# Kernel tuning notes

Hardware: AMD Instinct MI355X
Metric: run time of the kernel (lower is better)

Reference implementation:

```python
import math
import jax, jax.numpy as jnp
import numpy as np

D = 1024
NH = 16
DH = D // NH


def setup_inputs() -> dict:
    key = jax.random.key(0)
    k1, k2, k3 = jax.random.split(key, 3)
    x = jax.random.normal(k1, (2, 2048, D), dtype=jnp.float32)
    s = 1.0 / math.sqrt(D)
    W_qkv = jax.random.normal(k2, (D, 3 * D), dtype=jnp.float32) * s
    W_o = jax.random.normal(k3, (D, D), dtype=jnp.float32) * s
    return {"x": x, "W_qkv": W_qkv, "W_o": W_o}


def _rope(q, k, base=10000.0):
    # q, k: [B, H, T, dh]
    half = q.shape[-1] // 2
    freqs = jnp.arange(half, dtype=q.dtype) / half
    theta = 1.0 / base ** freqs                      # [half]
    t = jnp.arange(q.shape[-2], dtype=q.dtype)       # [T]
    ang = t[:, None] * theta[None, :]                # [T, half]
    cos = jnp.cos(ang)[None, None, :, :]
    sin = jnp.sin(ang)[None, None, :, :]

    def rot(x):
        x1, x2 = x[..., :half], x[..., half:]
        return jnp.concatenate([x1 * cos - x2 * sin, x1 * sin + x2 * cos], axis=-1)

    return rot(q), rot(k)


def reference(x, W_qkv, W_o):
    B, T, d = x.shape
    qkv = x @ W_qkv                                   # [B, T, 3D]
    q, k, v = jnp.split(qkv, 3, axis=-1)
    q = q.reshape(B, T, NH, DH).transpose(0, 2, 1, 3)  # [B, H, T, dh]
    k = k.reshape(B, T, NH, DH).transpose(0, 2, 1, 3)
    v = v.reshape(B, T, NH, DH).transpose(0, 2, 1, 3)
    q, k = _rope(q, k)
    att = jnp.einsum('bhtd,bhsd->bhts', q, k) / math.sqrt(DH)  # [B, H, T, T]
    mask = jnp.triu(jnp.full((T, T), -jnp.inf, dtype=att.dtype), 1)
    att = att + mask
    w = jax.nn.softmax(att, axis=-1)
    y = jnp.einsum('bhts,bhsd->bhtd', w, v)           # [B, H, T, dh]
    y = y.transpose(0, 2, 1, 3).reshape(B, T, d)
    return y @ W_o
```

## Files before the change

### kernel.cpp

```cpp
#include <hip/hip_runtime.h>

typedef __bf16 bf16x8 __attribute__((ext_vector_type(8)));
typedef float f32x4 __attribute__((ext_vector_type(4)));
typedef float f32x16 __attribute__((ext_vector_type(16)));

constexpr int SEQ = 2048;
constexpr int DMODEL = 1024;

#define GLL(gp, lp)                                                              \
  __builtin_amdgcn_global_load_lds((const __attribute__((address_space(1))) void*)(gp), \
                                   (__attribute__((address_space(3))) void*)(lp), 16, 0, 0)

__global__ __launch_bounds__(256) void prep_kernel(const float* __restrict__ x,
                                                   const float* __restrict__ Wqkv,
                                                   const float* __restrict__ Wo,
                                                   __bf16* __restrict__ xbf,
                                                   __bf16* __restrict__ WqkvT,
                                                   __bf16* __restrict__ WoT,
                                                   float2* __restrict__ sct) {
  __shared__ __bf16 tile[64][72];
  int blk = blockIdx.x, t = threadIdx.x;

  if (blk < 256) {
    int i = blk * 256 + t;
    int tt = i >> 5, j = i & 31;
    float theta = exp2f(-(float)j * 0.41524101186092953f);
    float s, c;
    __sincosf((float)tt * theta, &s, &c);
    sct[i] = make_float2(c, s);
    return;
  }
  if (blk >= 1280) {
    size_t i = (size_t)(blk - 1280) * 256 + t;
    const float* sp = x + i * 8;
    float4 f0 = *reinterpret_cast<const float4*>(sp);
    float4 f1 = *reinterpret_cast<const float4*>(sp + 4);
    alignas(16) __bf16 tmp[8];
    tmp[0] = (__bf16)f0.x; tmp[1] = (__bf16)f0.y; tmp[2] = (__bf16)f0.z; tmp[3] = (__bf16)f0.w;
    tmp[4] = (__bf16)f1.x; tmp[5] = (__bf16)f1.y; tmp[6] = (__bf16)f1.z; tmp[7] = (__bf16)f1.w;
    *reinterpret_cast<uint4*>(xbf + i * 8) = *reinterpret_cast<const uint4*>(tmp);
    return;
  }
  const float* src;
  __bf16* dst;
  int C, R, c0, r0;
  if (blk < 512) {
    int idx = blk - 256;
    src = Wo; dst = WoT; R = 1024; C = 1024;
    c0 = (idx & 15) * 64; r0 = (idx >> 4) * 64;
  } else {
    int idx = blk - 512;
    src = Wqkv; dst = WqkvT; R = 1024; C = 3072;
    c0 = (idx % 48) * 64; r0 = (idx / 48) * 64;
  }
#pragma unroll
  for (int p = 0; p < 2; ++p) {
    int flat = p * 256 + t;
    int i = flat >> 3;
    int j8 = (flat & 7) * 8;
    const float* sp = &src[(size_t)(r0 + i) * C + c0 + j8];
    float4 f0 = *reinterpret_cast<const float4*>(sp);
    float4 f1 = *reinterpret_cast<const float4*>(sp + 4);
    tile[i][j8 + 0] = (__bf16)f0.x; tile[i][j8 + 1] = (__bf16)f0.y;
    tile[i][j8 + 2] = (__bf16)f0.z; tile[i][j8 + 3] = (__bf16)f0.w;
    tile[i][j8 + 4] = (__bf16)f1.x; tile[i][j8 + 5] = (__bf16)f1.y;
    tile[i][j8 + 6] = (__bf16)f1.z; tile[i][j8 + 7] = (__bf16)f1.w;
  }
  __syncthreads();
#pragma unroll
  for (int p = 0; p < 2; ++p) {
    int flat = p * 256 + t;
    int i = flat >> 3;
    int j8 = (flat & 7) * 8;
    alignas(16) __bf16 tmp[8];
#pragma unroll
    for (int jj = 0; jj < 8; ++jj) tmp[jj] = tile[j8 + jj][i];
    *reinterpret_cast<uint4*>(&dst[(size_t)(c0 + i) * R + r0 + j8]) =
        *reinterpret_cast<const uint4*>(tmp);
  }
}

__global__ __launch_bounds__(256) void transpose_v(const __bf16* __restrict__ qkv,
                                                   __bf16* __restrict__ vt) {
  __shared__ __bf16 tile[64][72];
  int s0 = blockIdx.x * 64;
  int bh = blockIdx.y;
  int b = bh >> 4, h = bh & 15;
  const __bf16* src = qkv + (size_t)b * SEQ * 3072 + 2048 + h * 64;
  __bf16* dst = vt + (size_t)bh * 64 * SEQ;
  int t = threadIdx.x;
#pragma unroll
  for (int p = 0; p < 2; ++p) {
    int flat = p * 256 + t;
    int i = flat >> 3;
    int j8 = (flat & 7) * 8;
    *reinterpret_cast<uint4*>(&tile[i][j8]) =
        *reinterpret_cast<const uint4*>(src + (size_t)(s0 + i) * 3072 + j8);
  }
  __syncthreads();
#pragma unroll
  for (int p = 0; p < 2; ++p) {
    int flat = p * 256 + t;
    int i = flat >> 3;
    int j8 = (flat & 7) * 8;
    alignas(16) __bf16 tmp[8];
#pragma unroll
    for (int jj = 0; jj < 8; ++jj) tmp[jj] = tile[j8 + jj][i];
    *reinterpret_cast<uint4*>(dst + (size_t)i * SEQ + s0 + j8) =
        *reinterpret_cast<const uint4*>(tmp);
  }
}

template <typename CT, int BN, int MODE>
__global__ __launch_bounds__(256) void gemm_bt_lds(const __bf16* __restrict__ A,
                                                   const __bf16* __restrict__ BT,
                                                   CT* __restrict__ C,
                                                   int M, int N, int K, int lda, int ldc,
                                                   const float2* __restrict__ sct) {
  constexpr int MF = (BN == 128) ? 4 : 2;
  __shared__ __align__(16) __bf16 A_lds[128][64];
  __shared__ __align__(16) __bf16 B_lds[BN][64];
  int tid = threadIdx.x;
  int lane = tid & 63, w = tid >> 6;
  int g = lane >> 4, l15 = lane & 15;
  int wr = (BN == 128) ? (w >> 1) : w;
  int wc = (BN == 128) ? (w & 1) : 0;
  int m0 = blockIdx.x * 128;
  int n0 = blockIdx.y * BN;
  int srow = lane >> 3, scol = (lane & 7) * 8;

  const __bf16* ag = A + (size_t)(m0 + w * 32 + srow) * lda + scol;
  const __bf16* bg = BT + (size_t)(n0 + w * (BN / 4) + srow) * K + scol;

  f32x4 acc[MF][4] = {};

  for (int k0 = 0; k0 < K; k0 += 64) {
    __syncthreads();
#pragma unroll
    for (int i = 0; i < 4; ++i)
      GLL(ag + (size_t)(i * 8) * lda + k0, &A_lds[w * 32 + i * 8][0]);
#pragma unroll
    for (int i = 0; i < BN / 32; ++i)
      GLL(bg + (size_t)(i * 8) * K + k0, &B_lds[w * (BN / 4) + i * 8][0]);
    __syncthreads();
#pragma unroll
    for (int kk = 0; kk < 2; ++kk) {
      bf16x8 a[MF], bb[4];
#pragma unroll
      for (int m = 0; m < MF; ++m)
        a[m] = *reinterpret_cast<const bf16x8*>(&A_lds[wr * (MF * 16) + m * 16 + l15][kk * 32 + g * 8]);
#pragma unroll
      for (int n = 0; n < 4; ++n)
        bb[n] = *reinterpret_cast<const bf16x8*>(&B_lds[wc * 64 + n * 16 + l15][kk * 32 + g * 8]);
#pragma unroll
      for (int m = 0; m < MF; ++m)
#pragma unroll
        for (int n = 0; n < 4; ++n)
          acc[m][n] = __builtin_amdgcn_mfma_f32_16x16x32_bf16(a[m], bb[n], acc[m][n], 0, 0, 0);
    }
  }

  if constexpr (MODE == 1) {
    bool isq = (n0 < 1024), isk = (n0 >= 1024 && n0 < 2048);
    if (isq || isk) {
      float sc = isq ? 0.18033688011112042f : 1.0f;
#pragma unroll
      for (int m = 0; m < MF; ++m)
#pragma unroll
        for (int r = 0; r < 4; ++r) {
          int row = m0 + wr * (MF * 16) + m * 16 + 4 * g + r;
          int t = row & (SEQ - 1);
#pragma unroll
          for (int n = 0; n < 2; ++n) {
            int j = n * 16 + l15;
            float2 cs = sct[(t << 5) + j];
            float x1 = acc[m][n][r], x2 = acc[m][n + 2][r];
            acc[m][n][r]     = (x1 * cs.x - x2 * cs.y) * sc;
            acc[m][n + 2][r] = (x1 * cs.y + x2 * cs.x) * sc;
          }
        }
    }
  }

#pragma unroll
  for (int m = 0; m < MF; ++m)
#pragma unroll
    for (int n = 0; n < 4; ++n)
#pragma unroll
      for (int r = 0; r < 4; ++r) {
        int row = m0 + wr * (MF * 16) + m * 16 + 4 * g + r;
        int col = n0 + wc * 64 + n * 16 + l15;
        C[(size_t)row * ldc + col] = (CT)acc[m][n][r];
      }
}

__device__ inline uint32_t pkbf(float a, float b) {
  union { __bf16 h[2]; uint32_t u; } z;
  z.h[0] = (__bf16)a; z.h[1] = (__bf16)b;
  return z.u;
}

__global__ __launch_bounds__(128, 3) void attn_kernel(__bf16* __restrict__ qkv,
                                                      const __bf16* __restrict__ vt,
                                                      float* __restrict__ pml) {
  __shared__ __align__(16) __bf16 K_lds[2][64][64];

  int tid = threadIdx.x;
  int w = tid >> 6, lane = tid & 63;
  int l31 = lane & 31, hi = lane >> 5;
  int bid = blockIdx.x;
  int it = bid >> 5, bh = bid & 31;
  int b = bh >> 4, h = bh & 15;

  int qc, kv0, kv1, half;
  bool split;
  if (it < 32) {
    qc = 31 - (it >> 1);
    half = it & 1;
    int NTf = qc + 1;
    int hs = (NTf + 1) >> 1;
    kv0 = half ? hs : 0;
    kv1 = half ? NTf : hs;
    split = true;
  } else {
    qc = 47 - it;
    kv0 = 0;
    kv1 = qc + 1;
    split = false;
    half = 0;
  }
  int NT = kv1 - kv0;

  __bf16* qbase = qkv + (size_t)b * SEQ * 3072 + h * 64;
  const __bf16* kbase = qbase + 1024;
  const __bf16* vtb = vt + (size_t)bh * 64 * SEQ;

  int q_g = qc * 64 + w * 32 + l31;

  int r8 = lane >> 3;
  int cxe = 8 * ((lane & 7) ^ r8);

  auto STAGE = [&](int bufv, int t) {
#pragma unroll
    for (int i = 0; i < 4; ++i) {
      int R = w * 32 + i * 8;
      GLL(kbase + (size_t)(t * 64 + R + r8) * 3072 + cxe, &K_lds[bufv][R][0]);
    }
  };

  bf16x8 qf[4];
#pragma unroll
  for (int ds = 0; ds < 4; ++ds)
    qf[ds] = *reinterpret_cast<const bf16x8*>(qbase + (size_t)q_g * 3072 + ds * 16 + 8 * hi);

  f32x16 oacc[2] = {};
  float m_run = -1e30f, l_run = 0.f;

  STAGE(0, kv0);
  __syncthreads();

  int buf = 0;
  for (int jb = 0; jb < NT; ++jb) {
    int kt_g = kv0 + jb;
    bool pre = (jb + 1 < NT);
    if (pre) STAGE(buf ^ 1, kt_g + 1);

    uint4 vr[8];
#pragma unroll
    for (int dt = 0; dt < 2; ++dt)
#pragma unroll
      for (int ks = 0; ks < 4; ++ks)
        vr[dt * 4 + ks] = *reinterpret_cast<const uint4*>(
            vtb + (size_t)(dt * 32 + l31) * SEQ + kt_g * 64 + ks * 16 + 8 * hi);

    f32x16 sacc[2] = {};
    __builtin_amdgcn_s_setprio(1);
#pragma unroll
    for (int kt = 0; kt < 2; ++kt) {
#pragma unroll
      for (int ds = 0; ds < 4; ++ds) {
        bf16x8 kf = *reinterpret_cast<const bf16x8*>(
            &K_lds[buf][kt * 32 + l31][(ds * 16 + 8 * hi) ^ ((l31 & 7) * 8)]);
        sacc[kt] = __builtin_amdgcn_mfma_f32_32x32x16_bf16(kf, qf[ds], sacc[kt], 0, 0, 0);
      }
    }
    __builtin_amdgcn_s_setprio(0);

    if (kt_g == qc) {
#pragma unroll
      for (int kt = 0; kt < 2; ++kt)
#pragma unroll
        for (int r = 0; r < 16; ++r) {
          int k_g = kt_g * 64 + kt * 32 + (r & 3) + 8 * (r >> 2) + 4 * hi;
          if (k_g > q_g) sacc[kt][r] = -1e30f;
        }
    }

    float mx[8];
#pragma unroll
    for (int r = 0; r < 8; ++r)
      mx[r] = fmaxf(fmaxf(sacc[0][r], sacc[0][r + 8]), fmaxf(sacc[1][r], sacc[1][r + 8]));
    float m01 = fmaxf(fmaxf(mx[0], mx[1]), fmaxf(mx[2], mx[3]));
    float m23 = fmaxf(fmaxf(mx[4], mx[5]), fmaxf(mx[6], mx[7]));
    float tm = fmaxf(m01, m23);
    tm = fmaxf(tm, __shfl_xor(tm, 32));

    float m_new, alpha;
    if (__all(tm - m_run <= 8.f)) {
      m_new = m_run;
      alpha = 1.f;
    } else {
      m_new = fmaxf(m_run, tm);
      alpha = exp2f(m_run - m_new);
      m_run = m_new;
#pragma unroll
      for (int dt = 0; dt < 2; ++dt)
#pragma unroll
        for (int r = 0; r < 16; ++r) oacc[dt][r] *= alpha;
    }

    float s0 = 0.f, s1 = 0.f, s2 = 0.f, s3 = 0.f;
#pragma unroll
    for (int kt = 0; kt < 2; ++kt) {
#pragma unroll
      for (int r = 0; r < 16; r += 4) {
        float p0 = exp2f(sacc[kt][r + 0] - m_new);
        float p1 = exp2f(sacc[kt][r + 1] - m_new);
        float p2 = exp2f(sacc[kt][r + 2] - m_new);
        float p3 = exp2f(sacc[kt][r + 3] - m_new);
        sacc[kt][r + 0] = p0; sacc[kt][r + 1] = p1;
        sacc[kt][r + 2] = p2; sacc[kt][r + 3] = p3;
        s0 += p0; s1 += p1; s2 += p2; s3 += p3;
      }
    }
    float sum = (s0 + s1) + (s2 + s3);
    sum += __shfl_xor(sum, 32);
    l_run = l_run * alpha + sum;

    uint4 pa[4];
#pragma unroll
    for (int ks = 0; ks < 4; ++ks) {
      int v0 = 2 * ks, v1 = v0 + 1;
      int t0 = v0 >> 2, rb0 = 4 * (v0 & 3);
      int t1 = v1 >> 2, rb1 = 4 * (v1 & 3);
      uint32_t a01, a23, b01, b23;
      if (t0 == 0) { a01 = pkbf(sacc[0][rb0 + 0], sacc[0][rb0 + 1]);
                     a23 = pkbf(sacc[0][rb0 + 2], sacc[0][rb0 + 3]); }
      else         { a01 = pkbf(sacc[1][rb0 + 0], sacc[1][rb0 + 1]);
                     a23 = pkbf(sacc[1][rb0 + 2], sacc[1][rb0 + 3]); }
      if (t1 == 0) { b01 = pkbf(sacc[0][rb1 + 0], sacc[0][rb1 + 1]);
                     b23 = pkbf(sacc[0][rb1 + 2], sacc[0][rb1 + 3]); }
      else         { b01 = pkbf(sacc[1][rb1 + 0], sacc[1][rb1 + 1]);
                     b23 = pkbf(sacc[1][rb1 + 2], sacc[1][rb1 + 3]); }
      uint32_t t01 = hi ? a01 : b01;
      uint32_t t23 = hi ? a23 : b23;
      uint32_t r01 = __shfl_xor(t01, 32);
      uint32_t r23 = __shfl_xor(t23, 32);
      uint32_t k01 = hi ? b01 : a01;
      uint32_t k23 = hi ? b23 : a23;
      pa[ks].x = hi ? r01 : k01;
      pa[ks].y = hi ? r23 : k23;
      pa[ks].z = hi ? k01 : r01;
      pa[ks].w = hi ? k23 : r23;
    }

    __builtin_amdgcn_s_setprio(1);
#pragma unroll
    for (int dt = 0; dt < 2; ++dt) {
#pragma unroll
      for (int ks = 0; ks < 4; ++ks) {
        oacc[dt] = __builtin_amdgcn_mfma_f32_32x32x16_bf16(
            *reinterpret_cast<const bf16x8*>(&vr[dt * 4 + ks]),
            *reinterpret_cast<const bf16x8*>(&pa[ks]), oacc[dt], 0, 0, 0);
      }
    }
    __builtin_amdgcn_s_setprio(0);

    if (pre) {
      asm volatile("s_waitcnt vmcnt(0)" ::: "memory");
      __syncthreads();
    }
    buf ^= 1;
  }

  if (!split) {
    float inv = 1.0f / l_run;
#pragma unroll
    for (int dt = 0; dt < 2; ++dt)
#pragma unroll
      for (int u = 0; u < 4; ++u) {
        int d0 = dt * 32 + 8 * u + 4 * hi;
        alignas(8) __bf16 tmp[4];
#pragma unroll
        for (int m = 0; m < 4; ++m) tmp[m] = (__bf16)(oacc[dt][4 * u + m] * inv);
        *reinterpret_cast<uint2*>(qbase + (size_t)q_g * 3072 + d0) =
            *reinterpret_cast<const uint2*>(tmp);
      }
  } else {
    int item = ((qc - 16) * 2 + half) * 32 + bh;
    int q_local = w * 32 + l31;
    __bf16* pobase = qkv + (size_t)(item * 4 + (q_local >> 4)) * 3072 + 2048 + (q_local & 15) * 64;
#pragma unroll
    for (int dt = 0; dt < 2; ++dt)
#pragma unroll
      for (int u = 0; u < 4; ++u) {
        int d0 = dt * 32 + 8 * u + 4 * hi;
        alignas(8) __bf16 tmp[4];
#pragma unroll
        for (int m = 0; m < 4; ++m) tmp[m] = (__bf16)oacc[dt][4 * u + m];
        *reinterpret_cast<uint2*>(pobase + d0) = *reinterpret_cast<const uint2*>(tmp);
      }
    if (hi == 0) {
      pml[item * 128 + q_local] = m_run;
      pml[item * 128 + 64 + q_local] = l_run;
    }
  }
}

__global__ __launch_bounds__(128) void combine_kernel(__bf16* __restrict__ qkv,
                                                      const float* __restrict__ pml) {
  int bid = blockIdx.x;
  int qc = 16 + (bid >> 5), bh = bid & 31;
  int b = bh >> 4, h = bh & 15;
  int t = threadIdx.x;
  int q = t >> 1, dh = (t & 1) * 32;

  int i0 = ((qc - 16) * 2 + 0) * 32 + bh;
  int i1 = i0 + 32;
  float m0 = pml[i0 * 128 + q], l0 = pml[i0 * 128 + 64 + q];
  float m1 = pml[i1 * 128 + q], l1 = pml[i1 * 128 + 64 + q];
  float M = fmaxf(m0, m1);
  float w0 = exp2f(m0 - M), w1 = exp2f(m1 - M);
  float inv = 1.0f / (l0 * w0 + l1 * w1);

  const __bf16* p0 = qkv + (size_t)(i0 * 4 + (q >> 4)) * 3072 + 2048 + (q & 15) * 64 + dh;
  const __bf16* p1 = qkv + (size_t)(i1 * 4 + (q >> 4)) * 3072 + 2048 + (q & 15) * 64 + dh;
  __bf16* yq = qkv + (size_t)(b * SEQ + qc * 64 + q) * 3072 + h * 64 + dh;

#pragma unroll
  for (int c = 0; c < 4; ++c) {
    uint4 ua = *reinterpret_cast<const uint4*>(p0 + c * 8);
    uint4 ub = *reinterpret_cast<const uint4*>(p1 + c * 8);
    const __bf16* va = reinterpret_cast<const __bf16*>(&ua);
    const __bf16* vb = reinterpret_cast<const __bf16*>(&ub);
    alignas(16) __bf16 out[8];
#pragma unroll
    for (int j = 0; j < 8; ++j)
      out[j] = (__bf16)((((float)va[j]) * w0 + ((float)vb[j]) * w1) * inv);
    *reinterpret_cast<uint4*>(yq + c * 8) = *reinterpret_cast<const uint4*>(out);
  }
}

extern "C" void kernel_launch(void* const* d_in, const int* in_sizes, int n_in,
                              void* d_out, int out_size, void* d_ws, size_t ws_size,
                              hipStream_t stream) {
  const float* x = (const float*)d_in[0];
  const float* Wqkv = (const float*)d_in[1];
  const float* Wo = (const float*)d_in[2];
  float* out = (float*)d_out;

  __bf16* ws = (__bf16*)d_ws;
  __bf16* WqkvT = ws;
  __bf16* WoT = WqkvT + (size_t)3072 * 1024;
  __bf16* qkv = WoT + (size_t)1024 * 1024;
  __bf16* xbf = qkv + (size_t)4096 * 3072;
  __bf16* vtb = xbf + (size_t)4096 * 1024;
  float* pml = (float*)(vtb + (size_t)32 * 64 * SEQ);
  float2* sct = (float2*)(pml + 1024 * 128);

  prep_kernel<<<3328, 256, 0, stream>>>(x, Wqkv, Wo, xbf, WqkvT, WoT, sct);

  gemm_bt_lds<__bf16, 128, 1><<<dim3(32, 24), 256, 0, stream>>>(
      xbf, WqkvT, qkv, 4096, 3072, 1024, 1024, 3072, sct);

  transpose_v<<<dim3(32, 32), 256, 0, stream>>>(qkv, vtb);

  attn_kernel<<<1536, 128, 0, stream>>>(qkv, vtb, pml);
  combine_kernel<<<512, 128, 0, stream>>>(qkv, pml);

  gemm_bt_lds<float, 64, 0><<<dim3(32, 16), 256, 0, stream>>>(
      qkv, WoT, out, 4096, 1024, 1024, 3072, 1024, sct);
}
```

Measured before the change: 146.9 us.

## Balance causal attention work with fixed-size KV chunks and swizzle GEMM block order

Attention work is reorganised into 66 items of 8 KV tiles each, built from a compile-time map that packs consecutive query chunks' KV ranges into equal chunks. Query chunks whose range crosses a chunk boundary emit partial outputs that a generalised combine kernel merges, with up to five partials per chunk. Partial outputs are stored in dead workspace regions (xbf, WqkvT and a tail buffer) rather than a separate buffer. Separately, the GEMM kernels remap block IDs in an 8-way interleave to improve cache locality. The cost is more partial writes and combine traffic, plus extra syncs at segment boundaries inside a block.

```diff
diff --git a/kernel.cpp b/kernel.cpp
--- a/kernel.cpp
+++ b/kernel.cpp
@@ -10,6 +10,62 @@
 #define GLL(gp, lp)                                                              \
   __builtin_amdgcn_global_load_lds((const __attribute__((address_space(1))) void*)(gp), \
                                    (__attribute__((address_space(3))) void*)(lp), 16, 0, 0)
+
+constexpr int CHUNK = 8;
+constexpr int N_ITEMS = 66;
+constexpr int SEG_MAX = 4;
+constexpr int P_MAX = 5;
+struct AttnMaps {
+  short seg_qc[N_ITEMS][SEG_MAX];
+  short seg_j0[N_ITEMS][SEG_MAX];
+  short seg_len[N_ITEMS][SEG_MAX];
+  short seg_slot[N_ITEMS][SEG_MAX];
+  short seg_cnt[N_ITEMS];
+  short q_pcnt[32];
+  short q_pbase[32];
+  short n_slots;
+};
+constexpr AttnMaps buildMaps() {
+  AttnMaps m = {};
+  int pos = 0, slot = 0;
+  for (int qc = 31; qc >= 0; --qc) {
+    int len_total = qc + 1;
+    int start = pos;
+    bool full_one = (start / CHUNK) == ((start + len_total - 1) / CHUNK);
+    m.q_pbase[qc] = (short)slot;
+    int pc = 0;
+    int j = 0;
+    while (j < len_total) {
+      int p = start + j;
+      int it = p / CHUNK;
+      int room = CHUNK - (p % CHUNK);
+      int len = (len_total - j < room) ? (len_total - j) : room;
+      int s = m.seg_cnt[it]++;
+      m.seg_qc[it][s] = (short)qc;
+      m.seg_j0[it][s] = (short)j;
+      m.seg_len[it][s] = (short)len;
+      if (full_one) m.seg_slot[it][s] = (short)-1;
+      else { m.seg_slot[it][s] = (short)slot++; ++pc; }
+      j += len;
+    }
+    m.q_pcnt[qc] = (short)pc;
+    pos += len_total;
+  }
+  m.n_slots = (short)slot;
+  return m;
+}
+constexpr AttnMaps AM = buildMaps();
+static_assert(AM.n_slots == 90, "slot count");
+static_assert(AM.n_slots * 32 <= 2880, "slot capacity");
+
+__device__ inline __bf16* slot_ptr(int gs, __bf16* xbf, __bf16* wqkvt, __bf16* ptail) {
+  if (gs < 1024) return xbf + (size_t)gs * 4096;
+  if (gs < 1792) return wqkvt + (size_t)(gs - 1024) * 4096;
+  return ptail + (size_t)(gs - 1792) * 4096;
+}
+__device__ inline float* pml_ptr(__bf16* qkv, int gs) {
+  return (float*)(qkv + (size_t)(gs >> 2) * 3072 + 2048) + (gs & 3) * 128;
+}
 
 __global__ __launch_bounds__(256) void prep_kernel(const float* __restrict__ x,
                                                    const float* __restrict__ Wqkv,
@@ -125,8 +181,11 @@
   int g = lane >> 4, l15 = lane & 15;
   int wr = (BN == 128) ? (w >> 1) : w;
   int wc = (BN == 128) ? (w & 1) : 0;
-  int m0 = blockIdx.x * 128;
-  int n0 = blockIdx.y * BN;
+  int nwg = gridDim.x * gridDim.y;
+  int lid = blockIdx.y * gridDim.x + blockIdx.x;
+  int swz = (lid & 7) * (nwg >> 3) + (lid >> 3);
+  int m0 = (swz % gridDim.x) * 128;
+  int n0 = (swz / gridDim.x) * BN;
   int srow = lane >> 3, scol = (lane & 7) * 8;
 
   const __bf16* ag = A + (size_t)(m0 + w * 32 + srow) * lda + scol;
@@ -202,41 +261,22 @@
 
 __global__ __launch_bounds__(128, 3) void attn_kernel(__bf16* __restrict__ qkv,
                                                       const __bf16* __restrict__ vt,
-                                                      float* __restrict__ pml) {
+                                                      __bf16* __restrict__ xbf,
+                                                      __bf16* __restrict__ wqkvt,
+                                                      __bf16* __restrict__ ptail) {
   __shared__ __align__(16) __bf16 K_lds[2][64][64];
 
   int tid = threadIdx.x;
   int w = tid >> 6, lane = tid & 63;
   int l31 = lane & 31, hi = lane >> 5;
   int bid = blockIdx.x;
-  int it = bid >> 5, bh = bid & 31;
+  int item = bid >> 5, bh = bid & 31;
   int b = bh >> 4, h = bh & 15;
-
-  int qc, kv0, kv1, half;
-  bool split;
-  if (it < 32) {
-    qc = 31 - (it >> 1);
-    half = it & 1;
-    int NTf = qc + 1;
-    int hs = (NTf + 1) >> 1;
-    kv0 = half ? hs : 0;
-    kv1 = half ? NTf : hs;
-    split = true;
-  } else {
-    qc = 47 - it;
-    kv0 = 0;
-    kv1 = qc + 1;
-    split = false;
-    half = 0;
-  }
-  int NT = kv1 - kv0;
 
   __bf16* qbase = qkv + (size_t)b * SEQ * 3072 + h * 64;
   const __bf16* kbase = qbase + 1024;
   const __bf16* vtb = vt + (size_t)bh * 64 * SEQ;
 
-  int q_g = qc * 64 + w * 32 + l31;
-
   int r8 = lane >> 3;
   int cxe = 8 * ((lane & 7) ^ r8);
 
@@ -248,206 +288,238 @@
     }
   };
 
-  bf16x8 qf[4];
-#pragma unroll
-  for (int ds = 0; ds < 4; ++ds)
-    qf[ds] = *reinterpret_cast<const bf16x8*>(qbase + (size_t)q_g * 3072 + ds * 16 + 8 * hi);
-
-  f32x16 oacc[2] = {};
-  float m_run = -1e30f, l_run = 0.f;
-
-  STAGE(0, kv0);
-  __syncthreads();
-
-  int buf = 0;
-  for (int jb = 0; jb < NT; ++jb) {
-    int kt_g = kv0 + jb;
-    bool pre = (jb + 1 < NT);
-    if (pre) STAGE(buf ^ 1, kt_g + 1);
-
-    uint4 vr[8];
-#pragma unroll
-    for (int dt = 0; dt < 2; ++dt)
-#pragma unroll
-      for (int ks = 0; ks < 4; ++ks)
-        vr[dt * 4 + ks] = *reinterpret_cast<const uint4*>(
-            vtb + (size_t)(dt * 32 + l31) * SEQ + kt_g * 64 + ks * 16 + 8 * hi);
-
-    f32x16 sacc[2] = {};
-    __builtin_amdgcn_s_setprio(1);
-#pragma unroll
-    for (int kt = 0; kt < 2; ++kt) {
-#pragma unroll
-      for (int ds = 0; ds < 4; ++ds) {
-        bf16x8 kf = *reinterpret_cast<const bf16x8*>(
-            &K_lds[buf][kt * 32 + l31][(ds * 16 + 8 * hi) ^ ((l31 & 7) * 8)]);
-        sacc[kt] = __builtin_amdgcn_mfma_f32_32x32x16_bf16(kf, qf[ds], sacc[kt], 0, 0, 0);
-      }
-    }
-    __builtin_amdgcn_s_setprio(0);
-
-    if (kt_g == qc) {
-#pragma unroll
-      for (int kt = 0; kt < 2; ++kt)
-#pragma unroll
-        for (int r = 0; r < 16; ++r) {
-          int k_g = kt_g * 64 + kt * 32 + (r & 3) + 8 * (r >> 2) + 4 * hi;
-          if (k_g > q_g) sacc[kt][r] = -1e30f;
+  int nseg = AM.seg_cnt[item];
+  for (int sg = 0; sg < nseg; ++sg) {
+    int qc = AM.seg_qc[item][sg];
+    int j0 = AM.seg_j0[item][sg];
+    int NT = AM.seg_len[item][sg];
+    int slot = AM.seg_slot[item][sg];
+
+    int q_g = qc * 64 + w * 32 + l31;
+
+    bf16x8 qf[4];
+#pragma unroll
+    for (int ds = 0; ds < 4; ++ds)
+      qf[ds] = *reinterpret_cast<const bf16x8*>(qbase + (size_t)q_g * 3072 + ds * 16 + 8 * hi);
+
+    f32x16 oacc[2] = {};
+    float m_run = -1e30f, l_run = 0.f;
+
+    __syncthreads();
+    STAGE(0, j0);
+    __syncthreads();
+
+    int buf = 0;
+    for (int jb = 0; jb < NT; ++jb) {
+      int kt_g = j0 + jb;
+      bool pre = (jb + 1 < NT);
+      if (pre) STAGE(buf ^ 1, kt_g + 1);
+
+      uint4 vr[8];
+#pragma unroll
+      for (int dt = 0; dt < 2; ++dt)
+#pragma unroll
+        for (int ks = 0; ks < 4; ++ks)
+          vr[dt * 4 + ks] = *reinterpret_cast<const uint4*>(
+              vtb + (size_t)(dt * 32 + l31) * SEQ + kt_g * 64 + ks * 16 + 8 * hi);
+
+      f32x16 sacc[2] = {};
+      __builtin_amdgcn_s_setprio(1);
+#pragma unroll
+      for (int kt = 0; kt < 2; ++kt) {
+#pragma unroll
+        for (int ds = 0; ds < 4; ++ds) {
+          bf16x8 kf = *reinterpret_cast<const bf16x8*>(
+              &K_lds[buf][kt * 32 + l31][(ds * 16 + 8 * hi) ^ ((l31 & 7) * 8)]);
+          sacc[kt] = __builtin_amdgcn_mfma_f32_32x32x16_bf16(kf, qf[ds], sacc[kt], 0, 0, 0);
         }
-    }
-
-    float mx[8];
-#pragma unroll
-    for (int r = 0; r < 8; ++r)
-      mx[r] = fmaxf(fmaxf(sacc[0][r], sacc[0][r + 8]), fmaxf(sacc[1][r], sacc[1][r + 8]));
-    float m01 = fmaxf(fmaxf(mx[0], mx[1]), fmaxf(mx[2], mx[3]));
-    float m23 = fmaxf(fmaxf(mx[4], mx[5]), fmaxf(mx[6], mx[7]));
-    float tm = fmaxf(m01, m23);
-    tm = fmaxf(tm, __shfl_xor(tm, 32));
-
-    float m_new, alpha;
-    if (__all(tm - m_run <= 8.f)) {
-      m_new = m_run;
-      alpha = 1.f;
+      }
+      __builtin_amdgcn_s_setprio(0);
+
+      if (kt_g == qc) {
+#pragma unroll
+        for (int kt = 0; kt < 2; ++kt)
+#pragma unroll
+          for (int r = 0; r < 16; ++r) {
+            int k_g = kt_g * 64 + kt * 32 + (r & 3) + 8 * (r >> 2) + 4 * hi;
+            if (k_g > q_g) sacc[kt][r] = -1e30f;
+          }
+      }
+
+      float mx[8];
+#pragma unroll
+      for (int r = 0; r < 8; ++r)
+        mx[r] = fmaxf(fmaxf(sacc[0][r], sacc[0][r + 8]), fmaxf(sacc[1][r], sacc[1][r + 8]));
+      float m01 = fmaxf(fmaxf(mx[0], mx[1]), fmaxf(mx[2], mx[3]));
+      float m23 = fmaxf(fmaxf(mx[4], mx[5]), fmaxf(mx[6], mx[7]));
+      float tm = fmaxf(m01, m23);
+      tm = fmaxf(tm, __shfl_xor(tm, 32));
+
+      float m_new, alpha;
+      if (__all(tm - m_run <= 8.f)) {
+        m_new = m_run;
+        alpha = 1.f;
+      } else {
+        m_new = fmaxf(m_run, tm);
+        alpha = exp2f(m_run - m_new);
+        m_run = m_new;
+#pragma unroll
+        for (int dt = 0; dt < 2; ++dt)
+#pragma unroll
+          for (int r = 0; r < 16; ++r) oacc[dt][r] *= alpha;
+      }
+
+      float s0 = 0.f, s1 = 0.f, s2 = 0.f, s3 = 0.f;
+#pragma unroll
+      for (int kt = 0; kt < 2; ++kt) {
+#pragma unroll
+        for (int r = 0; r < 16; r += 4) {
+          float p0 = exp2f(sacc[kt][r + 0] - m_new);
+          float p1 = exp2f(sacc[kt][r + 1] - m_new);
+          float p2 = exp2f(sacc[kt][r + 2] - m_new);
+          float p3 = exp2f(sacc[kt][r + 3] - m_new);
+          sacc[kt][r + 0] = p0; sacc[kt][r + 1] = p1;
+          sacc[kt][r + 2] = p2; sacc[kt][r + 3] = p3;
+          s0 += p0; s1 += p1; s2 += p2; s3 += p3;
+        }
+      }
+      float sum = (s0 + s1) + (s2 + s3);
+      sum += __shfl_xor(sum, 32);
+      l_run = l_run * alpha + sum;
+
+      uint4 pa[4];
+#pragma unroll
+      for (int ks = 0; ks < 4; ++ks) {
+        int v0 = 2 * ks, v1 = v0 + 1;
+        int t0 = v0 >> 2, rb0 = 4 * (v0 & 3);
+        int t1 = v1 >> 2, rb1 = 4 * (v1 & 3);
+        uint32_t a01, a23, b01, b23;
+        if (t0 == 0) { a01 = pkbf(sacc[0][rb0 + 0], sacc[0][rb0 + 1]);
+                       a23 = pkbf(sacc[0][rb0 + 2], sacc[0][rb0 + 3]); }
+        else         { a01 = pkbf(sacc[1][rb0 + 0], sacc[1][rb0 + 1]);
+                       a23 = pkbf(sacc[1][rb0 + 2], sacc[1][rb0 + 3]); }
+        if (t1 == 0) { b01 = pkbf(sacc[0][rb1 + 0], sacc[0][rb1 + 1]);
+                       b23 = pkbf(sacc[0][rb1 + 2], sacc[0][rb1 + 3]); }
+        else         { b01 = pkbf(sacc[1][rb1 + 0], sacc[1][rb1 + 1]);
+                       b23 = pkbf(sacc[1][rb1 + 2], sacc[1][rb1 + 3]); }
+        uint32_t t01 = hi ? a01 : b01;
+        uint32_t t23 = hi ? a23 : b23;
+        uint32_t r01 = __shfl_xor(t01, 32);
+        uint32_t r23 = __shfl_xor(t23, 32);
+        uint32_t k01 = hi ? b01 : a01;
+        uint32_t k23 = hi ? b23 : a23;
+        pa[ks].x = hi ? r01 : k01;
+        pa[ks].y = hi ? r23 : k23;
+        pa[ks].z = hi ? k01 : r01;
+        pa[ks].w = hi ? k23 : r23;
+      }
+
+      __builtin_amdgcn_s_setprio(1);
+#pragma unroll
+      for (int dt = 0; dt < 2; ++dt) {
+#pragma unroll
+        for (int ks = 0; ks < 4; ++ks) {
+          oacc[dt] = __builtin_amdgcn_mfma_f32_32x32x16_bf16(
+              *reinterpret_cast<const bf16x8*>(&vr[dt * 4 + ks]),
+              *reinterpret_cast<const bf16x8*>(&pa[ks]), oacc[dt], 0, 0, 0);
+        }
+      }
+      __builtin_amdgcn_s_setprio(0);
+
+      if (pre) {
+        asm volatile("s_waitcnt vmcnt(0)" ::: "memory");
+        __syncthreads();
+      }
+      buf ^= 1;
+    }
+
+    int q_local = w * 32 + l31;
+    if (slot < 0) {
+      float inv = 1.0f / l_run;
+#pragma unroll
+      for (int dt = 0; dt < 2; ++dt)
+#pragma unroll
+        for (int u = 0; u < 4; ++u) {
+          int d0 = dt * 32 + 8 * u + 4 * hi;
+          alignas(8) __bf16 tmp[4];
+#pragma unroll
+          for (int m = 0; m < 4; ++m) tmp[m] = (__bf16)(oacc[dt][4 * u + m] * inv);
+          *reinterpret_cast<uint2*>(qbase + (size_t)q_g * 3072 + d0) =
+              *reinterpret_cast<const uint2*>(tmp);
+        }
     } else {
-      m_new = fmaxf(m_run, tm);
-      alpha = exp2f(m_run - m_new);
-      m_run = m_new;
+      int gs = slot * 32 + bh;
+      __bf16* pobase = slot_ptr(gs, xbf, wqkvt, ptail) + (size_t)q_local * 64;
 #pragma unroll
       for (int dt = 0; dt < 2; ++dt)
 #pragma unroll
-        for (int r = 0; r < 16; ++r) oacc[dt][r] *= alpha;
-    }
-
-    float s0 = 0.f, s1 = 0.f, s2 = 0.f, s3 = 0.f;
-#pragma unroll
-    for (int kt = 0; kt < 2; ++kt) {
-#pragma unroll
-      for (int r = 0; r < 16; r += 4) {
-        float p0 = exp2f(sacc[kt][r + 0] - m_new);
-        float p1 = exp2f(sacc[kt][r + 1] - m_new);
-        float p2 = exp2f(sacc[kt][r + 2] - m_new);
-        float p3 = exp2f(sacc[kt][r + 3] - m_new);
-        sacc[kt][r + 0] = p0; sacc[kt][r + 1] = p1;
-        sacc[kt][r + 2] = p2; sacc[kt][r + 3] = p3;
-        s0 += p0; s1 += p1; s2 += p2; s3 += p3;
-      }
-    }
-    float sum = (s0 + s1) + (s2 + s3);
-    sum += __shfl_xor(sum, 32);
-    l_run = l_run * alpha + sum;
-
-    uint4 pa[4];
-#pragma unroll
-    for (int ks = 0; ks < 4; ++ks) {
-      int v0 = 2 * ks, v1 = v0 + 1;
-      int t0 = v0 >> 2, rb0 = 4 * (v0 & 3);
-      int t1 = v1 >> 2, rb1 = 4 * (v1 & 3);
-      uint32_t a01, a23, b01, b23;
-      if (t0 == 0) { a01 = pkbf(sacc[0][rb0 + 0], sacc[0][rb0 + 1]);
-                     a23 = pkbf(sacc[0][rb0 + 2], sacc[0][rb0 + 3]); }
-      else         { a01 = pkbf(sacc[1][rb0 + 0], sacc[1][rb0 + 1]);
-                     a23 = pkbf(sacc[1][rb0 + 2], sacc[1][rb0 + 3]); }
-      if (t1 == 0) { b01 = pkbf(sacc[0][rb1 + 0], sacc[0][rb1 + 1]);
-                     b23 = pkbf(sacc[0][rb1 + 2], sacc[0][rb1 + 3]); }
-      else         { b01 = pkbf(sacc[1][rb1 + 0], sacc[1][rb1 + 1]);
-                     b23 = pkbf(sacc[1][rb1 + 2], sacc[1][rb1 + 3]); }
-      uint32_t t01 = hi ? a01 : b01;
-      uint32_t t23 = hi ? a23 : b23;
-      uint32_t r01 = __shfl_xor(t01, 32);
-      uint32_t r23 = __shfl_xor(t23, 32);
-      uint32_t k01 = hi ? b01 : a01;
-      uint32_t k23 = hi ? b23 : a23;
-      pa[ks].x = hi ? r01 : k01;
-      pa[ks].y = hi ? r23 : k23;
-      pa[ks].z = hi ? k01 : r01;
-      pa[ks].w = hi ? k23 : r23;
-    }
-
-    __builtin_amdgcn_s_setprio(1);
-#pragma unroll
-    for (int dt = 0; dt < 2; ++dt) {
-#pragma unroll
-      for (int ks = 0; ks < 4; ++ks) {
-        oacc[dt] = __builtin_amdgcn_mfma_f32_32x32x16_bf16(
-            *reinterpret_cast<const bf16x8*>(&vr[dt * 4 + ks]),
-            *reinterpret_cast<const bf16x8*>(&pa[ks]), oacc[dt], 0, 0, 0);
-      }
-    }
-    __builtin_amdgcn_s_setprio(0);
-
-    if (pre) {
-      asm volatile("s_waitcnt vmcnt(0)" ::: "memory");
-      __syncthreads();
-    }
-    buf ^= 1;
-  }
-
-  if (!split) {
-    float inv = 1.0f / l_run;
-#pragma unroll
-    for (int dt = 0; dt < 2; ++dt)
-#pragma unroll
-      for (int u = 0; u < 4; ++u) {
-        int d0 = dt * 32 + 8 * u + 4 * hi;
-        alignas(8) __bf16 tmp[4];
-#pragma unroll
-        for (int m = 0; m < 4; ++m) tmp[m] = (__bf16)(oacc[dt][4 * u + m] * inv);
-        *reinterpret_cast<uint2*>(qbase + (size_t)q_g * 3072 + d0) =
-            *reinterpret_cast<const uint2*>(tmp);
-      }
-  } else {
-    int item = ((qc - 16) * 2 + half) * 32 + bh;
-    int q_local = w * 32 + l31;
-    __bf16* pobase = qkv + (size_t)(item * 4 + (q_local >> 4)) * 3072 + 2048 + (q_local & 15) * 64;
-#pragma unroll
-    for (int dt = 0; dt < 2; ++dt)
-#pragma unroll
-      for (int u = 0; u < 4; ++u) {
-        int d0 = dt * 32 + 8 * u + 4 * hi;
-        alignas(8) __bf16 tmp[4];
-#pragma unroll
-        for (int m = 0; m < 4; ++m) tmp[m] = (__bf16)oacc[dt][4 * u + m];
-        *reinterpret_cast<uint2*>(pobase + d0) = *reinterpret_cast<const uint2*>(tmp);
-      }
-    if (hi == 0) {
-      pml[item * 128 + q_local] = m_run;
-      pml[item * 128 + 64 + q_local] = l_run;
+        for (int u = 0; u < 4; ++u) {
+          int d0 = dt * 32 + 8 * u + 4 * hi;
+          alignas(8) __bf16 tmp[4];
+#pragma unroll
+          for (int m = 0; m < 4; ++m) tmp[m] = (__bf16)oacc[dt][4 * u + m];
+          *reinterpret_cast<uint2*>(pobase + d0) = *reinterpret_cast<const uint2*>(tmp);
+        }
+      if (hi == 0) {
+        float* pm = pml_ptr(qkv, gs);
+        pm[q_local] = m_run;
+        pm[64 + q_local] = l_run;
+      }
     }
   }
 }
 
 __global__ __launch_bounds__(128) void combine_kernel(__bf16* __restrict__ qkv,
-                                                      const float* __restrict__ pml) {
+                                                      __bf16* __restrict__ xbf,
+                                                      __bf16* __restrict__ wqkvt,
+                                                      __bf16* __restrict__ ptail) {
   int bid = blockIdx.x;
-  int qc = 16 + (bid >> 5), bh = bid & 31;
+  int qc = bid >> 5, bh = bid & 31;
+  int p = AM.q_pcnt[qc];
+  if (p == 0) return;
+  int base = AM.q_pbase[qc];
   int b = bh >> 4, h = bh & 15;
   int t = threadIdx.x;
   int q = t >> 1, dh = (t & 1) * 32;
 
-  int i0 = ((qc - 16) * 2 + 0) * 32 + bh;
-  int i1 = i0 + 32;
-  float m0 = pml[i0 * 128 + q], l0 = pml[i0 * 128 + 64 + q];
-  float m1 = pml[i1 * 128 + q], l1 = pml[i1 * 128 + 64 + q];
-  float M = fmaxf(m0, m1);
-  float w0 = exp2f(m0 - M), w1 = exp2f(m1 - M);
-  float inv = 1.0f / (l0 * w0 + l1 * w1);
-
-  const __bf16* p0 = qkv + (size_t)(i0 * 4 + (q >> 4)) * 3072 + 2048 + (q & 15) * 64 + dh;
-  const __bf16* p1 = qkv + (size_t)(i1 * 4 + (q >> 4)) * 3072 + 2048 + (q & 15) * 64 + dh;
+  float mv[P_MAX], lv[P_MAX], wgt[P_MAX];
+  float M = -1e30f;
+#pragma unroll
+  for (int i = 0; i < P_MAX; ++i) {
+    if (i < p) {
+      const float* pm = pml_ptr(qkv, (base + i) * 32 + bh);
+      mv[i] = pm[q];
+      lv[i] = pm[64 + q];
+      M = fmaxf(M, mv[i]);
+    } else { mv[i] = -1e30f; lv[i] = 0.f; }
+  }
+  float wsum = 0.f;
+#pragma unroll
+  for (int i = 0; i < P_MAX; ++i) {
+    wgt[i] = (i < p) ? exp2f(mv[i] - M) : 0.f;
+    wsum += lv[i] * wgt[i];
+  }
+  float inv = 1.0f / wsum;
+
   __bf16* yq = qkv + (size_t)(b * SEQ + qc * 64 + q) * 3072 + h * 64 + dh;
-
 #pragma unroll
   for (int c = 0; c < 4; ++c) {
-    uint4 ua = *reinterpret_cast<const uint4*>(p0 + c * 8);
-    uint4 ub = *reinterpret_cast<const uint4*>(p1 + c * 8);
-    const __bf16* va = reinterpret_cast<const __bf16*>(&ua);
-    const __bf16* vb = reinterpret_cast<const __bf16*>(&ub);
-    alignas(16) __bf16 out[8];
-#pragma unroll
-    for (int j = 0; j < 8; ++j)
-      out[j] = (__bf16)((((float)va[j]) * w0 + ((float)vb[j]) * w1) * inv);
-    *reinterpret_cast<uint4*>(yq + c * 8) = *reinterpret_cast<const uint4*>(out);
+    float accv[8] = {};
+#pragma unroll
+    for (int i = 0; i < P_MAX; ++i) {
+      if (i < p) {
+        const __bf16* po = slot_ptr((base + i) * 32 + bh, xbf, wqkvt, ptail) +
+                           (size_t)q * 64 + dh + c * 8;
+        uint4 u = *reinterpret_cast<const uint4*>(po);
+        const __bf16* v = reinterpret_cast<const __bf16*>(&u);
+#pragma unroll
+        for (int j = 0; j < 8; ++j) accv[j] += (float)v[j] * wgt[i];
+      }
+    }
+    alignas(16) __bf16 outv[8];
+#pragma unroll
+    for (int j = 0; j < 8; ++j) outv[j] = (__bf16)(accv[j] * inv);
+    *reinterpret_cast<uint4*>(yq + c * 8) = *reinterpret_cast<const uint4*>(outv);
   }
 }
 
@@ -465,8 +537,8 @@
   __bf16* qkv = WoT + (size_t)1024 * 1024;
   __bf16* xbf = qkv + (size_t)4096 * 3072;
   __bf16* vtb = xbf + (size_t)4096 * 1024;
-  float* pml = (float*)(vtb + (size_t)32 * 64 * SEQ);
-  float2* sct = (float2*)(pml + 1024 * 128);
+  float2* sct = (float2*)(vtb + (size_t)32 * 64 * SEQ);
+  __bf16* ptail = (__bf16*)(sct + 2048 * 32);
 
   prep_kernel<<<3328, 256, 0, stream>>>(x, Wqkv, Wo, xbf, WqkvT, WoT, sct);
 
@@ -475,8 +547,8 @@
 
   transpose_v<<<dim3(32, 32), 256, 0, stream>>>(qkv, vtb);
 
-  attn_kernel<<<1536, 128, 0, stream>>>(qkv, vtb, pml);
-  combine_kernel<<<512, 128, 0, stream>>>(qkv, pml);
+  attn_kernel<<<N_ITEMS * 32, 128, 0, stream>>>(qkv, vtb, xbf, WqkvT, ptail);
+  combine_kernel<<<1024, 128, 0, stream>>>(qkv, xbf, WqkvT, ptail);
 
   gemm_bt_lds<float, 64, 0><<<dim3(32, 16), 256, 0, stream>>>(
       qkv, WoT, out, 4096, 1024, 1024, 3072, 1024, sct);
```

Result: slower. 167.4 us (+13.9%).

## Fuse V transpose into QKV GEMM epilogue and combine into attention kernel

Applied to the files above, without the earlier changes.

The QKV GEMM epilogue now writes V tiles transposed through LDS directly into the vt buffer and skips the row-major V store. The separate transpose kernel is removed. The split-KV combine kernel is folded into the attention kernel: an atomic counter per (query chunk, head) lets the second-finishing half merge both partial results. This removes two kernel launches and an extra pass over V, at the cost of extra fences, an atomic per split block, and more LDS in the GEMM.

```diff
diff --git a/kernel.cpp b/kernel.cpp
--- a/kernel.cpp
+++ b/kernel.cpp
@@ -17,7 +17,8 @@
                                                    __bf16* __restrict__ xbf,
                                                    __bf16* __restrict__ WqkvT,
                                                    __bf16* __restrict__ WoT,
-                                                   float2* __restrict__ sct) {
+                                                   float2* __restrict__ sct,
+                                                   int* __restrict__ cnt) {
   __shared__ __bf16 tile[64][72];
   int blk = blockIdx.x, t = threadIdx.x;
 
@@ -28,6 +29,7 @@
     float s, c;
     __sincosf((float)tt * theta, &s, &c);
     sct[i] = make_float2(c, s);
+    if (i < 512) cnt[i] = 0;
     return;
   }
   if (blk >= 1280) {
@@ -80,43 +82,13 @@
   }
 }
 
-__global__ __launch_bounds__(256) void transpose_v(const __bf16* __restrict__ qkv,
-                                                   __bf16* __restrict__ vt) {
-  __shared__ __bf16 tile[64][72];
-  int s0 = blockIdx.x * 64;
-  int bh = blockIdx.y;
-  int b = bh >> 4, h = bh & 15;
-  const __bf16* src = qkv + (size_t)b * SEQ * 3072 + 2048 + h * 64;
-  __bf16* dst = vt + (size_t)bh * 64 * SEQ;
-  int t = threadIdx.x;
-#pragma unroll
-  for (int p = 0; p < 2; ++p) {
-    int flat = p * 256 + t;
-    int i = flat >> 3;
-    int j8 = (flat & 7) * 8;
-    *reinterpret_cast<uint4*>(&tile[i][j8]) =
-        *reinterpret_cast<const uint4*>(src + (size_t)(s0 + i) * 3072 + j8);
-  }
-  __syncthreads();
-#pragma unroll
-  for (int p = 0; p < 2; ++p) {
-    int flat = p * 256 + t;
-    int i = flat >> 3;
-    int j8 = (flat & 7) * 8;
-    alignas(16) __bf16 tmp[8];
-#pragma unroll
-    for (int jj = 0; jj < 8; ++jj) tmp[jj] = tile[j8 + jj][i];
-    *reinterpret_cast<uint4*>(dst + (size_t)i * SEQ + s0 + j8) =
-        *reinterpret_cast<const uint4*>(tmp);
-  }
-}
-
 template <typename CT, int BN, int MODE>
 __global__ __launch_bounds__(256) void gemm_bt_lds(const __bf16* __restrict__ A,
                                                    const __bf16* __restrict__ BT,
                                                    CT* __restrict__ C,
                                                    int M, int N, int K, int lda, int ldc,
-                                                   const float2* __restrict__ sct) {
+                                                   const float2* __restrict__ sct,
+                                                   __bf16* __restrict__ vt) {
   constexpr int MF = (BN == 128) ? 4 : 2;
   __shared__ __align__(16) __bf16 A_lds[128][64];
   __shared__ __align__(16) __bf16 B_lds[BN][64];
@@ -160,26 +132,56 @@
     }
   }
 
-  if constexpr (MODE == 1) {
-    bool isq = (n0 < 1024), isk = (n0 >= 1024 && n0 < 2048);
-    if (isq || isk) {
-      float sc = isq ? 0.18033688011112042f : 1.0f;
-#pragma unroll
-      for (int m = 0; m < MF; ++m)
-#pragma unroll
-        for (int r = 0; r < 4; ++r) {
-          int row = m0 + wr * (MF * 16) + m * 16 + 4 * g + r;
-          int t = row & (SEQ - 1);
-#pragma unroll
-          for (int n = 0; n < 2; ++n) {
-            int j = n * 16 + l15;
-            float2 cs = sct[(t << 5) + j];
-            float x1 = acc[m][n][r], x2 = acc[m][n + 2][r];
-            acc[m][n][r]     = (x1 * cs.x - x2 * cs.y) * sc;
-            acc[m][n + 2][r] = (x1 * cs.y + x2 * cs.x) * sc;
-          }
+  if constexpr (MODE == 3) {
+    if (n0 >= 2048) {
+      __shared__ __bf16 T_lds[128][72];
+      int b = m0 >> 11;
+      int s_base = m0 & (SEQ - 1);
+#pragma unroll
+      for (int half = 0; half < 2; ++half) {
+        __syncthreads();
+        if (wc == half) {
+#pragma unroll
+          for (int m = 0; m < MF; ++m)
+#pragma unroll
+            for (int n = 0; n < 4; ++n)
+#pragma unroll
+              for (int r = 0; r < 4; ++r)
+                T_lds[wr * 64 + m * 16 + 4 * g + r][n * 16 + l15] = (__bf16)acc[m][n][r];
         }
-    }
+        __syncthreads();
+        int head = ((n0 - 2048) >> 6) + half;
+        int bh = b * 16 + head;
+        int d = tid >> 2;
+        int s8 = (tid & 3) * 32;
+        __bf16* dst = vt + (size_t)bh * 64 * SEQ + (size_t)d * SEQ + s_base + s8;
+#pragma unroll
+        for (int j = 0; j < 4; ++j) {
+          alignas(16) __bf16 tmp[8];
+#pragma unroll
+          for (int e = 0; e < 8; ++e) tmp[e] = T_lds[s8 + j * 8 + e][d];
+          *reinterpret_cast<uint4*>(dst + j * 8) = *reinterpret_cast<const uint4*>(tmp);
+        }
+      }
+      return;
+    }
+    bool isq = (n0 < 1024);
+    float sc = isq ? 0.18033688011112042f : 1.0f;
+#pragma unroll
+    for (int m = 0; m < MF; ++m)
+#pragma unroll
+      for (int r = 0; r < 4; ++r) {
+        int row = m0 + wr * (MF * 16) + m * 16 + 4 * g + r;
+        int t = row & (SEQ - 1);
+#pragma unroll
+        for (int n = 0; n < 2; ++n) {
+          int j = n * 16 + l15;
+          float2 cs = sct[(t << 5) + j];
+          float x1 = acc[m][n][r], x2 = acc[m][n + 2][r];
+          acc[m][n][r]     = (x1 * cs.x - x2 * cs.y) * sc;
+          acc[m][n + 2][r] = (x1 * cs.y + x2 * cs.x) * sc;
+        }
+      }
   }
 
 #pragma unroll
@@ -202,8 +204,10 @@
 
 __global__ __launch_bounds__(128, 3) void attn_kernel(__bf16* __restrict__ qkv,
                                                       const __bf16* __restrict__ vt,
-                                                      float* __restrict__ pml) {
+                                                      float* __restrict__ pml,
+                                                      int* __restrict__ cnt) {
   __shared__ __align__(16) __bf16 K_lds[2][64][64];
+  __shared__ int do_comb;
 
   int tid = threadIdx.x;
   int w = tid >> 6, lane = tid & 63;
@@ -414,40 +418,41 @@
       pml[item * 128 + q_local] = m_run;
       pml[item * 128 + 64 + q_local] = l_run;
     }
-  }
-}
-
-__global__ __launch_bounds__(128) void combine_kernel(__bf16* __restrict__ qkv,
-                                                      const float* __restrict__ pml) {
-  int bid = blockIdx.x;
-  int qc = 16 + (bid >> 5), bh = bid & 31;
-  int b = bh >> 4, h = bh & 15;
-  int t = threadIdx.x;
-  int q = t >> 1, dh = (t & 1) * 32;
-
-  int i0 = ((qc - 16) * 2 + 0) * 32 + bh;
-  int i1 = i0 + 32;
-  float m0 = pml[i0 * 128 + q], l0 = pml[i0 * 128 + 64 + q];
-  float m1 = pml[i1 * 128 + q], l1 = pml[i1 * 128 + 64 + q];
-  float M = fmaxf(m0, m1);
-  float w0 = exp2f(m0 - M), w1 = exp2f(m1 - M);
-  float inv = 1.0f / (l0 * w0 + l1 * w1);
-
-  const __bf16* p0 = qkv + (size_t)(i0 * 4 + (q >> 4)) * 3072 + 2048 + (q & 15) * 64 + dh;
-  const __bf16* p1 = qkv + (size_t)(i1 * 4 + (q >> 4)) * 3072 + 2048 + (q & 15) * 64 + dh;
-  __bf16* yq = qkv + (size_t)(b * SEQ + qc * 64 + q) * 3072 + h * 64 + dh;
-
-#pragma unroll
-  for (int c = 0; c < 4; ++c) {
-    uint4 ua = *reinterpret_cast<const uint4*>(p0 + c * 8);
-    uint4 ub = *reinterpret_cast<const uint4*>(p1 + c * 8);
-    const __bf16* va = reinterpret_cast<const __bf16*>(&ua);
-    const __bf16* vb = reinterpret_cast<const __bf16*>(&ub);
-    alignas(16) __bf16 out[8];
-#pragma unroll
-    for (int j = 0; j < 8; ++j)
-      out[j] = (__bf16)((((float)va[j]) * w0 + ((float)vb[j]) * w1) * inv);
-    *reinterpret_cast<uint4*>(yq + c * 8) = *reinterpret_cast<const uint4*>(out);
+
+    __threadfence();
+    __syncthreads();
+    if (tid == 0) {
+      int old = atomicAdd(&cnt[(qc - 16) * 32 + bh], 1);
+      do_comb = (old == 1);
+    }
+    __syncthreads();
+    if (do_comb) {
+      __threadfence();
+      int q = tid >> 1, dh = (tid & 1) * 32;
+      int i0 = ((qc - 16) * 2 + 0) * 32 + bh;
+      int i1 = i0 + 32;
+      float m0 = pml[i0 * 128 + q], l0 = pml[i0 * 128 + 64 + q];
+      float m1 = pml[i1 * 128 + q], l1 = pml[i1 * 128 + 64 + q];
+      float M = fmaxf(m0, m1);
+      float w0 = exp2f(m0 - M), w1 = exp2f(m1 - M);
+      float inv = 1.0f / (l0 * w0 + l1 * w1);
+
+      const __bf16* p0 = qkv + (size_t)(i0 * 4 + (q >> 4)) * 3072 + 2048 + (q & 15) * 64 + dh;
+      const __bf16* p1 = qkv + (size_t)(i1 * 4 + (q >> 4)) * 3072 + 2048 + (q & 15) * 64 + dh;
+      __bf16* yq = qkv + (size_t)(b * SEQ + qc * 64 + q) * 3072 + h * 64 + dh;
+#pragma unroll
+      for (int c = 0; c < 4; ++c) {
+        uint4 ua = *reinterpret_cast<const uint4*>(p0 + c * 8);
+        uint4 ub = *reinterpret_cast<const uint4*>(p1 + c * 8);
+        const __bf16* va = reinterpret_cast<const __bf16*>(&ua);
+        const __bf16* vb = reinterpret_cast<const __bf16*>(&ub);
+        alignas(16) __bf16 outv[8];
+#pragma unroll
+        for (int j = 0; j < 8; ++j)
+          outv[j] = (__bf16)((((float)va[j]) * w0 + ((float)vb[j]) * w1) * inv);
+        *reinterpret_cast<uint4*>(yq + c * 8) = *reinterpret_cast<const uint4*>(outv);
+      }
+    }
   }
 }
 
@@ -467,17 +472,15 @@
   __bf16* vtb = xbf + (size_t)4096 * 1024;
   float* pml = (float*)(vtb + (size_t)32 * 64 * SEQ);
   float2* sct = (float2*)(pml + 1024 * 128);
-
-  prep_kernel<<<3328, 256, 0, stream>>>(x, Wqkv, Wo, xbf, WqkvT, WoT, sct);
-
-  gemm_bt_lds<__bf16, 128, 1><<<dim3(32, 24), 256, 0, stream>>>(
-      xbf, WqkvT, qkv, 4096, 3072, 1024, 1024, 3072, sct);
-
-  transpose_v<<<dim3(32, 32), 256, 0, stream>>>(qkv, vtb);
-
-  attn_kernel<<<1536, 128, 0, stream>>>(qkv, vtb, pml);
-  combine_kernel<<<512, 128, 0, stream>>>(qkv, pml);
+  int* cnt = (int*)(sct + 2048 * 32);
+
+  prep_kernel<<<3328, 256, 0, stream>>>(x, Wqkv, Wo, xbf, WqkvT, WoT, sct, cnt);
+
+  gemm_bt_lds<__bf16, 128, 3><<<dim3(32, 24), 256, 0, stream>>>(
+      xbf, WqkvT, qkv, 4096, 3072, 1024, 1024, 3072, sct, vtb);
+
+  attn_kernel<<<1536, 128, 0, stream>>>(qkv, vtb, pml, cnt);
 
   gemm_bt_lds<float, 64, 0><<<dim3(32, 16), 256, 0, stream>>>(
-      qkv, WoT, out, 4096, 1024, 1024, 3072, 1024, sct);
+      qkv, WoT, out, 4096, 1024, 1024, 3072, 1024, sct, nullptr);
 }
```

Result: slower. 250.5 us (+70.4%).
